# Optimization experiments

Hardware: AMD Instinct MI355X
Metric: run time of the kernel (lower is better)

Reference implementation:

```python
import jax, jax.numpy as jnp
import numpy as np
import math

D_MODEL = 512
N_HEADS = 8
MAX_SPAN = 512
SPAN_LOSS_COEF = 2e-4
NEG_INF = -1.0e9
R_SIZE = 4.0


def soft_span_mask(span, max_span, seq_len):
    # span: (H,) clamped span fractions
    i_idx = jnp.arange(seq_len, dtype=span.dtype)[:, None]
    j_idx = jnp.arange(seq_len, dtype=span.dtype)[None, :]
    dist = i_idx - j_idx                                  # (T, T)
    eff_span = (span * max_span)[:, None, None]           # (H, 1, 1)
    x = eff_span - dist[None, :, :]                       # (H, T, T)
    R = jnp.clip((x + 1.0) / R_SIZE, 0.0, 1.0)
    causal_ok = dist[None, :, :] >= 0
    log_R = jnp.maximum(jnp.log(R + 1e-10), NEG_INF)
    return jnp.where(causal_ok & (R > 0), log_R, NEG_INF)  # (H, T, T)


def setup_inputs() -> dict:
    key = jax.random.key(0)
    ks = jax.random.split(key, 6)
    B, T, D = 4, 2048, D_MODEL
    w_scale = 0.02
    return {
        "x": jax.random.normal(ks[0], (B, T, D), dtype=jnp.float32),
        "wq": jax.random.normal(ks[1], (D, D), dtype=jnp.float32) * w_scale,
        "wk": jax.random.normal(ks[2], (D, D), dtype=jnp.float32) * w_scale,
        "wv": jax.random.normal(ks[3], (D, D), dtype=jnp.float32) * w_scale,
        "wo": jax.random.normal(ks[4], (D, D), dtype=jnp.float32) * w_scale,
        "span_params": jax.random.uniform(ks[5], (N_HEADS,), dtype=jnp.float32),
    }


def reference(x, wq, wk, wv, wo, span_params):
    B, T, D = x.shape
    H = N_HEADS
    d_h = D // H

    clamped_span = jnp.clip(span_params, 0.0, 1.0)

    # nn.Linear(bias=False): y = x @ W.T
    Q = (x @ wq.T).reshape(B, T, H, d_h).transpose(0, 2, 1, 3)  # (B,H,T,dh)
    K = (x @ wk.T).reshape(B, T, H, d_h).transpose(0, 2, 1, 3)
    V = (x @ wv.T).reshape(B, T, H, d_h).transpose(0, 2, 1, 3)

    scale = 1.0 / math.sqrt(d_h)
    scores = jnp.einsum("bhqd,bhkd->bhqk", Q, K) * scale        # (B,H,T,T)
    scores = scores + soft_span_mask(clamped_span, MAX_SPAN, T)[None]

    weights = jax.nn.softmax(scores, axis=-1)
    out = jnp.einsum("bhqk,bhkd->bhqd", weights, V)             # (B,H,T,dh)
    out = out.transpose(0, 2, 1, 3).reshape(B, T, D)
    output = out @ wo.T

    span_loss = SPAN_LOSS_COEF * clamped_span.mean()
    return output, span_loss
```

## Files before the change

kernel.cpp:

```cpp
#include <hip/hip_runtime.h>
#include <math.h>

#define T_SEQ   2048
#define DMODEL  512
#define NHEADS  8
#define DH      64
#define NEG_INF -1.0e9f

typedef __attribute__((ext_vector_type(8))) short short8;
typedef __attribute__((ext_vector_type(4))) float f32x4;
typedef unsigned int u32;
typedef unsigned short u16;

__device__ __forceinline__ u16 f2bf(float f) {
    union { float f; u32 u; } w; w.f = f;
    return (u16)((w.u + 0x8000u) >> 16);
}

__device__ __forceinline__ void async_load16(const u16* g, u16* l) {
    __builtin_amdgcn_global_load_lds(
        (const __attribute__((address_space(1))) u32*)(const void*)g,
        (__attribute__((address_space(3))) u32*)(void*)l, 16, 0, 0);
}

__global__ void cast_all(const float* __restrict__ x,  const float* __restrict__ wq,
                         const float* __restrict__ wk, const float* __restrict__ wv,
                         const float* __restrict__ wo, const float* __restrict__ sp,
                         u16* __restrict__ xb,  u16* __restrict__ wqb,
                         u16* __restrict__ wkb, u16* __restrict__ wvb,
                         u16* __restrict__ wob, float* __restrict__ loss_out)
{
    const int bid = blockIdx.x;
    const float* src; u16* dst; int i;
    if (bid < 4096) { src = x; dst = xb; i = bid * 256 + threadIdx.x; }
    else {
        const int wsel = (bid - 4096) >> 8;
        src = (wsel == 0) ? wq : (wsel == 1) ? wk : (wsel == 2) ? wv : wo;
        dst = (wsel == 0) ? wqb : (wsel == 1) ? wkb : (wsel == 2) ? wvb : wob;
        i = ((bid - 4096) & 255) * 256 + threadIdx.x;
    }
    float4 v = ((const float4*)src)[i];
    ushort4 o;
    o.x = f2bf(v.x); o.y = f2bf(v.y); o.z = f2bf(v.z); o.w = f2bf(v.w);
    ((ushort4*)dst)[i] = o;
    if (bid == 5119 && threadIdx.x == 0) {
        float s = 0.0f;
        for (int h = 0; h < NHEADS; ++h)
            s += fminf(fmaxf(sp[h], 0.0f), 1.0f);
        loss_out[0] = 2e-4f * (s * 0.125f);
    }
}

__global__ __launch_bounds__(256)
void gemm_bf16(const u16* __restrict__ A,
               const u16* __restrict__ W0, const u16* __restrict__ W1,
               const u16* __restrict__ W2,
               u16* __restrict__ Cb0, u16* __restrict__ Cb1,
               u16* __restrict__ Cb2,
               float* __restrict__ Cf, int scatter)
{
    constexpr int K = 512, BK = 64;
    const u16* W  = (blockIdx.z == 0) ? W0 : (blockIdx.z == 1) ? W1 : W2;
    u16*       Cb = (blockIdx.z == 0) ? Cb0 : (blockIdx.z == 1) ? Cb1 : Cb2;

    __shared__ __align__(16) u16 smem[16384];
    u16* As = smem;
    u16* Bs = smem + 8192;

    const int t    = threadIdx.x;
    const int lane = t & 63;
    const int wave = t >> 6;
    const int wm   = wave >> 1, wn = wave & 1;
    const int m0   = blockIdx.x * 128, n0 = blockIdx.y * 128;

    const int srow = t >> 3;
    const int kb   = (t & 7) ^ (srow & 7);
    const u16* gA = A + (size_t)(m0 + srow) * K + kb * 8;
    const u16* gW = W + (size_t)(n0 + srow) * K + kb * 8;

    const int rA = wm * 64 + (lane & 15);
    const int rB = wn * 64 + (lane & 15);
    const int kq = lane >> 4;
    const int offA0 = rA * BK + ((kq      ^ (rA & 7)) * 8);
    const int offA1 = rA * BK + (((4 + kq) ^ (rA & 7)) * 8);
    const int offB0 = rB * BK + ((kq      ^ (rB & 7)) * 8);
    const int offB1 = rB * BK + (((4 + kq) ^ (rB & 7)) * 8);

    f32x4 acc[4][4];
#pragma unroll
    for (int it = 0; it < 4; ++it)
#pragma unroll
        for (int jt = 0; jt < 4; ++jt) acc[it][jt] = (f32x4)0.0f;

    for (int k0 = 0; k0 < K; k0 += BK) {
        __syncthreads();
#pragma unroll
        for (int i = 0; i < 4; ++i) {
            async_load16(gA + k0 + i * (32 * K), As + t * 8 + i * 2048);
            async_load16(gW + k0 + i * (32 * K), Bs + t * 8 + i * 2048);
        }
        __syncthreads();

        short8 af[4][2], bfr[4][2];
#pragma unroll
        for (int it = 0; it < 4; ++it) {
            af[it][0]  = *(const short8*)(As + offA0 + it * 16 * BK);
            af[it][1]  = *(const short8*)(As + offA1 + it * 16 * BK);
            bfr[it][0] = *(const short8*)(Bs + offB0 + it * 16 * BK);
            bfr[it][1] = *(const short8*)(Bs + offB1 + it * 16 * BK);
        }
#pragma unroll
        for (int it = 0; it < 4; ++it)
#pragma unroll
            for (int jt = 0; jt < 4; ++jt) {
                acc[it][jt] = __builtin_amdgcn_mfma_f32_16x16x32_bf16(
                    af[it][0], bfr[jt][0], acc[it][jt], 0, 0, 0);
                acc[it][jt] = __builtin_amdgcn_mfma_f32_16x16x32_bf16(
                    af[it][1], bfr[jt][1], acc[it][jt], 0, 0, 0);
            }
    }

    const int r0 = (lane >> 4) * 4;
    const int cl = lane & 15;

    if (scatter) {
        const bool vt_mode = (blockIdx.z == 2);
        constexpr int P = 136;
#pragma unroll
        for (int rnd = 0; rnd < 2; ++rnd) {
            __syncthreads();
#pragma unroll
            for (int s = 0; s < 2; ++s) {
                const int it = rnd * 2 + s;
                const int lrow = wm * 32 + s * 16 + r0;
#pragma unroll
                for (int jt = 0; jt < 4; ++jt) {
                    const int cc = wn * 64 + jt * 16 + cl;
#pragma unroll
                    for (int r = 0; r < 4; ++r)
                        smem[(lrow + r) * P + cc] = f2bf(acc[it][jt][r]);
                }
            }
            __syncthreads();
            if (!vt_mode) {
                const int lrow2 = t >> 2;
                const int h2    = (t >> 1) & 1;
                const int dhalf = t & 1;
                const int grow  = m0 + (lrow2 >> 5) * 64 + rnd * 32 + (lrow2 & 31);
                const int b     = grow >> 11, tt = grow & 2047;
                const int h     = (n0 >> 6) + h2;
                u16* dst = Cb + ((size_t)((b * NHEADS + h) * T_SEQ + tt)) * DH + dhalf * 32;
                const u16* srcl = smem + lrow2 * P + h2 * 64 + dhalf * 32;
#pragma unroll
                for (int i = 0; i < 4; ++i)
                    ((uint4*)dst)[i] = *(const uint4*)(srcl + i * 8);
            } else {
                const int hd   = t >> 1;
                const int run  = t & 1;
                const int h    = (n0 >> 6) + (hd >> 6);
                const int d    = hd & 63;
                const int tb   = m0 + run * 64 + rnd * 32;
                const int b    = tb >> 11;
                u16* dst = Cb + (((size_t)(b * NHEADS + h) * DH + d) << 11) + (tb & 2047);
                union { uint4 v[4]; u16 s[32]; } pk;
#pragma unroll
                for (int i = 0; i < 32; ++i)
                    pk.s[i] = smem[(run * 32 + i) * P + hd];
#pragma unroll
                for (int i = 0; i < 4; ++i)
                    ((uint4*)dst)[i] = pk.v[i];
            }
        }
    } else {
#pragma unroll
        for (int it = 0; it < 4; ++it) {
#pragma unroll
            for (int r = 0; r < 4; ++r) {
                const int row = m0 + wm * 64 + it * 16 + r0 + r;
#pragma unroll
                for (int jt = 0; jt < 4; ++jt) {
                    const int col = n0 + wn * 64 + jt * 16 + cl;
                    Cf[(size_t)row * DMODEL + col] = acc[it][jt][r];
                }
            }
        }
    }
}

__global__ __launch_bounds__(64, 2)
void attn_wave(const u16* __restrict__ Q, const u16* __restrict__ K,
               const u16* __restrict__ Vt, const float* __restrict__ span_params,
               u16* __restrict__ out)
{
    __shared__ __align__(16) u16 Ps[16 * 72];

    const int lane = threadIdx.x;
    const int nl   = lane & 15;
    const int quad = lane >> 4;
    const int xi   = blockIdx.x;
    const int b    = xi >> 3;
    const int h    = ((xi & 7) + 5 * b) & 7;
    const int bh   = b * NHEADS + h;
    const int q0   = blockIdx.y * 16;

    const u16* Qh = Q  + (size_t)bh * (T_SEQ * DH);
    const u16* Kh = K  + (size_t)bh * (T_SEQ * DH);
    const u16* Vh = Vt + (size_t)bh * (DH * T_SEQ);

    float span = span_params[h];
    span = fminf(fmaxf(span, 0.0f), 1.0f);
    const float eff_span = span * 512.0f;
    const int wspan = (int)(eff_span + 1.0f) + 1;

    short8 qf0 = *(const short8*)(Qh + (size_t)(q0 + nl) * DH + quad * 8);
    short8 qf1 = *(const short8*)(Qh + (size_t)(q0 + nl) * DH + 32 + quad * 8);

    f32x4 o[4];
    float m_r[4], l_r[4];
#pragma unroll
    for (int d = 0; d < 4; ++d) o[d] = (f32x4)0.0f;
#pragma unroll
    for (int r = 0; r < 4; ++r) { m_r[r] = -1.0e30f; l_r[r] = 0.0f; }

    int j_lo = q0 - wspan;
    if (j_lo < 0) j_lo = 0;
    j_lo &= ~63;
    const int j_hi = (q0 + 15) & ~63;

    for (int j0 = j_lo; j0 <= j_hi; j0 += 64) {
        bool any[4];
#pragma unroll
        for (int n = 0; n < 4; ++n) {
            const int jn = j0 + n * 16;
            any[n] = (jn <= q0 + 15) &&
                     ((float)(q0 - jn - 15) < eff_span + 1.0f);
        }

        f32x4 s[4];
#pragma unroll
        for (int n = 0; n < 4; ++n) {
            s[n] = (f32x4)0.0f;
            if (any[n]) {
                const u16* kp = Kh + (size_t)(j0 + n * 16 + nl) * DH + quad * 8;
                short8 b0 = *(const short8*)kp;
                short8 b1 = *(const short8*)(kp + 32);
                s[n] = __builtin_amdgcn_mfma_f32_16x16x32_bf16(qf0, b0, s[n], 0, 0, 0);
                s[n] = __builtin_amdgcn_mfma_f32_16x16x32_bf16(qf1, b1, s[n], 0, 0, 0);
            }
        }

        const bool kf0 = any[0] | any[1];
        const bool kf1 = any[2] | any[3];
        short8 vb0[4], vb1[4];
#pragma unroll
        for (int d = 0; d < 4; ++d) {
            const u16* vp = Vh + (size_t)(d * 16 + nl) * T_SEQ + j0 + quad * 8;
            if (kf0) vb0[d] = *(const short8*)vp;
            if (kf1) vb1[d] = *(const short8*)(vp + 32);
        }

        float tmax[4] = {-1.0e30f, -1.0e30f, -1.0e30f, -1.0e30f};
#pragma unroll
        for (int n = 0; n < 4; ++n) {
            if (!any[n]) continue;
            const int jn = j0 + n * 16;
            const bool causal_b = (jn + 15 > q0);
            const bool span_b   = ((float)(q0 + 15 - jn) > eff_span - 3.0f);
            if (!causal_b && !span_b) {
#pragma unroll
                for (int r = 0; r < 4; ++r) {
                    const float sv = s[n][r] * 0.125f;
                    s[n][r] = sv;
                    tmax[r] = fmaxf(tmax[r], sv);
                }
            } else if (!span_b) {
#pragma unroll
                for (int r = 0; r < 4; ++r) {
                    const int dist = (q0 + quad * 4 + r) - (jn + nl);
                    const float sv = (dist >= 0) ? s[n][r] * 0.125f : NEG_INF;
                    s[n][r] = sv;
                    tmax[r] = fmaxf(tmax[r], sv);
                }
            } else {
#pragma unroll
                for (int r = 0; r < 4; ++r) {
                    const int dist = (q0 + quad * 4 + r) - (jn + nl);
                    float sv = NEG_INF;
                    if (dist >= 0) {
                        float xv = eff_span - (float)dist;
                        float R  = fminf(fmaxf((xv + 1.0f) * 0.25f, 0.0f), 1.0f);
                        if (R > 0.0f)
                            sv = s[n][r] * 0.125f +
                                 ((R < 1.0f) ? __logf(R + 1e-10f) : 0.0f);
                    }
                    s[n][r] = sv;
                    tmax[r] = fmaxf(tmax[r], sv);
                }
            }
        }

        float alpha[4];
#pragma unroll
        for (int r = 0; r < 4; ++r) {
            float t = tmax[r];
            t = fmaxf(t, __shfl_xor(t, 1));
            t = fmaxf(t, __shfl_xor(t, 2));
            t = fmaxf(t, __shfl_xor(t, 4));
            t = fmaxf(t, __shfl_xor(t, 8));
            const float m_new = fmaxf(m_r[r], t);
            alpha[r] = __expf(m_r[r] - m_new);
            m_r[r] = m_new;
        }

        float psum[4] = {0.0f, 0.0f, 0.0f, 0.0f};
#pragma unroll
        for (int n = 0; n < 4; ++n) {
            if (any[n]) {
#pragma unroll
                for (int r = 0; r < 4; ++r) {
                    const float pv = __expf(s[n][r] - m_r[r]);
                    psum[r] += pv;
                    Ps[(quad * 4 + r) * 72 + n * 16 + nl] = f2bf(pv);
                }
            } else {
#pragma unroll
                for (int r = 0; r < 4; ++r)
                    Ps[(quad * 4 + r) * 72 + n * 16 + nl] = 0;
            }
        }
#pragma unroll
        for (int r = 0; r < 4; ++r) {
            float ps = psum[r];
            ps += __shfl_xor(ps, 1);
            ps += __shfl_xor(ps, 2);
            ps += __shfl_xor(ps, 4);
            ps += __shfl_xor(ps, 8);
            l_r[r] = l_r[r] * alpha[r] + ps;
#pragma unroll
            for (int d = 0; d < 4; ++d) o[d][r] *= alpha[r];
        }

        const u16* pb = Ps + nl * 72;
        short8 a0 = *(const short8*)(pb + quad * 8);
        short8 a1 = *(const short8*)(pb + 32 + quad * 8);
#pragma unroll
        for (int d = 0; d < 4; ++d) {
            if (kf0)
                o[d] = __builtin_amdgcn_mfma_f32_16x16x32_bf16(a0, vb0[d], o[d], 0, 0, 0);
            if (kf1)
                o[d] = __builtin_amdgcn_mfma_f32_16x16x32_bf16(a1, vb1[d], o[d], 0, 0, 0);
        }
    }

#pragma unroll
    for (int r = 0; r < 4; ++r) {
        const int qg = q0 + quad * 4 + r;
        const float inv_l = 1.0f / l_r[r];
        u16* op = out + (size_t)(b * T_SEQ + qg) * DMODEL + h * 64;
#pragma unroll
        for (int d = 0; d < 4; ++d)
            op[d * 16 + nl] = f2bf(o[d][r] * inv_l);
    }
}

extern "C" void kernel_launch(void* const* d_in, const int* in_sizes, int n_in,
                              void* d_out, int out_size, void* d_ws, size_t ws_size,
                              hipStream_t stream)
{
    (void)in_sizes; (void)n_in; (void)out_size; (void)ws_size;
    const float* x  = (const float*)d_in[0];
    const float* wq = (const float*)d_in[1];
    const float* wk = (const float*)d_in[2];
    const float* wv = (const float*)d_in[3];
    const float* wo = (const float*)d_in[4];
    const float* sp = (const float*)d_in[5];
    float* out = (float*)d_out;

    const size_t elems = (size_t)4 * T_SEQ * DMODEL;
    u16* xb  = (u16*)d_ws;
    u16* Qb  = xb  + elems;
    u16* Kb  = Qb  + elems;
    u16* Vtb = Kb  + elems;
    u16* Ab  = Vtb + elems;
    u16* wqb = Ab  + elems;
    u16* wkb = wqb + 262144;
    u16* wvb = wkb + 262144;
    u16* wob = wvb + 262144;

    cast_all<<<5120, 256, 0, stream>>>(x, wq, wk, wv, wo, sp,
                                       xb, wqb, wkb, wvb, wob, out + elems);
    gemm_bf16<<<dim3(64, 4, 3), 256, 0, stream>>>(
        xb, wqb, wkb, wvb, Qb, Kb, Vtb, nullptr, 1);
    attn_wave<<<dim3(32, 128), 64, 0, stream>>>(Qb, Kb, Vtb, sp, Ab);
    gemm_bf16<<<dim3(64, 4, 1), 256, 0, stream>>>(
        Ab, wob, wob, wob, nullptr, nullptr, nullptr, out, 0);
}
```

Before: 176.4 us.

## Compute V transposed via swapped GEMM operands and pack four query waves per attention block

The V projection now runs as a separate GEMM with the operands swapped (Wv times x^T). Its output tile is already in the d-by-T orientation, so the epilogue writes contiguous 16-byte runs instead of gathering a strided column out of shared memory. The attention kernel now uses 256-thread blocks of four independent waves, each with its own P buffer, covering 64 queries. Blocks are issued in reverse query order so the longer causal tiles start first. This adds a kernel launch, and the V GEMM leans on indexing assumptions about the tile layout.

```diff
diff --git a/kernel.cpp b/kernel.cpp
--- a/kernel.cpp
+++ b/kernel.cpp
@@ -54,14 +54,12 @@
 __global__ __launch_bounds__(256)
 void gemm_bf16(const u16* __restrict__ A,
                const u16* __restrict__ W0, const u16* __restrict__ W1,
-               const u16* __restrict__ W2,
                u16* __restrict__ Cb0, u16* __restrict__ Cb1,
-               u16* __restrict__ Cb2,
-               float* __restrict__ Cf, int scatter)
+               float* __restrict__ Cf, int mode)
 {
     constexpr int K = 512, BK = 64;
-    const u16* W  = (blockIdx.z == 0) ? W0 : (blockIdx.z == 1) ? W1 : W2;
-    u16*       Cb = (blockIdx.z == 0) ? Cb0 : (blockIdx.z == 1) ? Cb1 : Cb2;
+    const u16* W  = (blockIdx.z == 0) ? W0 : W1;
+    u16*       Cb = (blockIdx.z == 0) ? Cb0 : Cb1;
 
     __shared__ __align__(16) u16 smem[16384];
     u16* As = smem;
@@ -123,55 +121,7 @@
     const int r0 = (lane >> 4) * 4;
     const int cl = lane & 15;
 
-    if (scatter) {
-        const bool vt_mode = (blockIdx.z == 2);
-        constexpr int P = 136;
-#pragma unroll
-        for (int rnd = 0; rnd < 2; ++rnd) {
-            __syncthreads();
-#pragma unroll
-            for (int s = 0; s < 2; ++s) {
-                const int it = rnd * 2 + s;
-                const int lrow = wm * 32 + s * 16 + r0;
-#pragma unroll
-                for (int jt = 0; jt < 4; ++jt) {
-                    const int cc = wn * 64 + jt * 16 + cl;
-#pragma unroll
-                    for (int r = 0; r < 4; ++r)
-                        smem[(lrow + r) * P + cc] = f2bf(acc[it][jt][r]);
-                }
-            }
-            __syncthreads();
-            if (!vt_mode) {
-                const int lrow2 = t >> 2;
-                const int h2    = (t >> 1) & 1;
-                const int dhalf = t & 1;
-                const int grow  = m0 + (lrow2 >> 5) * 64 + rnd * 32 + (lrow2 & 31);
-                const int b     = grow >> 11, tt = grow & 2047;
-                const int h     = (n0 >> 6) + h2;
-                u16* dst = Cb + ((size_t)((b * NHEADS + h) * T_SEQ + tt)) * DH + dhalf * 32;
-                const u16* srcl = smem + lrow2 * P + h2 * 64 + dhalf * 32;
-#pragma unroll
-                for (int i = 0; i < 4; ++i)
-                    ((uint4*)dst)[i] = *(const uint4*)(srcl + i * 8);
-            } else {
-                const int hd   = t >> 1;
-                const int run  = t & 1;
-                const int h    = (n0 >> 6) + (hd >> 6);
-                const int d    = hd & 63;
-                const int tb   = m0 + run * 64 + rnd * 32;
-                const int b    = tb >> 11;
-                u16* dst = Cb + (((size_t)(b * NHEADS + h) * DH + d) << 11) + (tb & 2047);
-                union { uint4 v[4]; u16 s[32]; } pk;
-#pragma unroll
-                for (int i = 0; i < 32; ++i)
-                    pk.s[i] = smem[(run * 32 + i) * P + hd];
-#pragma unroll
-                for (int i = 0; i < 4; ++i)
-                    ((uint4*)dst)[i] = pk.v[i];
-            }
-        }
-    } else {
+    if (mode == 2) {
 #pragma unroll
         for (int it = 0; it < 4; ++it) {
 #pragma unroll
@@ -184,24 +134,72 @@
                 }
             }
         }
-    }
-}
-
-__global__ __launch_bounds__(64, 2)
+        return;
+    }
+
+    constexpr int P = 136;
+#pragma unroll
+    for (int rnd = 0; rnd < 2; ++rnd) {
+        __syncthreads();
+#pragma unroll
+        for (int s = 0; s < 2; ++s) {
+            const int it = rnd * 2 + s;
+            const int lrow = wm * 32 + s * 16 + r0;
+#pragma unroll
+            for (int jt = 0; jt < 4; ++jt) {
+                const int cc = wn * 64 + jt * 16 + cl;
+#pragma unroll
+                for (int r = 0; r < 4; ++r)
+                    smem[(lrow + r) * P + cc] = f2bf(acc[it][jt][r]);
+            }
+        }
+        __syncthreads();
+        if (mode == 0) {
+            const int lrow2 = t >> 2;
+            const int h2    = (t >> 1) & 1;
+            const int dhalf = t & 1;
+            const int grow  = m0 + (lrow2 >> 5) * 64 + rnd * 32 + (lrow2 & 31);
+            const int b     = grow >> 11, tt = grow & 2047;
+            const int h     = (n0 >> 6) + h2;
+            u16* dst = Cb + ((size_t)((b * NHEADS + h) * T_SEQ + tt)) * DH + dhalf * 32;
+            const u16* srcl = smem + lrow2 * P + h2 * 64 + dhalf * 32;
+#pragma unroll
+            for (int i = 0; i < 4; ++i)
+                ((uint4*)dst)[i] = *(const uint4*)(srcl + i * 8);
+        } else {
+            const int rl = t >> 2;
+            const int q  = t & 3;
+            const int m  = m0 + (rl >> 5) * 64 + rnd * 32 + (rl & 31);
+            const int h  = m >> 6, d = m & 63;
+            const int n  = n0 + q * 32;
+            const int b  = n >> 11;
+            u16* dst = Cb + (((size_t)(b * NHEADS + h) * DH + d) << 11) + (n & 2047);
+            const u16* srcl = smem + rl * P + q * 32;
+            ((uint4*)dst)[0] = *(const uint4*)(srcl);
+            ((uint4*)dst)[1] = *(const uint4*)(srcl + 8);
+            ((uint4*)dst)[2] = *(const uint4*)(srcl + 16);
+            ((uint4*)dst)[3] = *(const uint4*)(srcl + 24);
+        }
+    }
+}
+
+__global__ __launch_bounds__(256)
 void attn_wave(const u16* __restrict__ Q, const u16* __restrict__ K,
                const u16* __restrict__ Vt, const float* __restrict__ span_params,
                u16* __restrict__ out)
 {
-    __shared__ __align__(16) u16 Ps[16 * 72];
-
-    const int lane = threadIdx.x;
+    __shared__ __align__(16) u16 Ps[4][16 * 72];
+
+    const int tid  = threadIdx.x;
+    const int lane = tid & 63;
+    const int w    = tid >> 6;
     const int nl   = lane & 15;
     const int quad = lane >> 4;
     const int xi   = blockIdx.x;
     const int b    = xi >> 3;
     const int h    = ((xi & 7) + 5 * b) & 7;
     const int bh   = b * NHEADS + h;
-    const int q0   = blockIdx.y * 16;
+    const int q0   = (31 - (int)blockIdx.y) * 64 + w * 16;
 
     const u16* Qh = Q  + (size_t)bh * (T_SEQ * DH);
     const u16* Kh = K  + (size_t)bh * (T_SEQ * DH);
@@ -320,12 +318,12 @@
                 for (int r = 0; r < 4; ++r) {
                     const float pv = __expf(s[n][r] - m_r[r]);
                     psum[r] += pv;
-                    Ps[(quad * 4 + r) * 72 + n * 16 + nl] = f2bf(pv);
+                    Ps[w][(quad * 4 + r) * 72 + n * 16 + nl] = f2bf(pv);
                 }
             } else {
 #pragma unroll
                 for (int r = 0; r < 4; ++r)
-                    Ps[(quad * 4 + r) * 72 + n * 16 + nl] = 0;
+                    Ps[w][(quad * 4 + r) * 72 + n * 16 + nl] = 0;
             }
         }
 #pragma unroll
@@ -340,7 +338,7 @@
             for (int d = 0; d < 4; ++d) o[d][r] *= alpha[r];
         }
 
-        const u16* pb = Ps + nl * 72;
+        const u16* pb = Ps[w] + nl * 72;
         short8 a0 = *(const short8*)(pb + quad * 8);
         short8 a1 = *(const short8*)(pb + 32 + quad * 8);
 #pragma unroll
@@ -389,9 +387,11 @@
 
     cast_all<<<5120, 256, 0, stream>>>(x, wq, wk, wv, wo, sp,
                                        xb, wqb, wkb, wvb, wob, out + elems);
-    gemm_bf16<<<dim3(64, 4, 3), 256, 0, stream>>>(
-        xb, wqb, wkb, wvb, Qb, Kb, Vtb, nullptr, 1);
-    attn_wave<<<dim3(32, 128), 64, 0, stream>>>(Qb, Kb, Vtb, sp, Ab);
+    gemm_bf16<<<dim3(64, 4, 2), 256, 0, stream>>>(
+        xb, wqb, wkb, Qb, Kb, nullptr, 0);
+    gemm_bf16<<<dim3(4, 64, 1), 256, 0, stream>>>(
+        wvb, xb, nullptr, Vtb, nullptr, nullptr, 1);
+    attn_wave<<<dim3(32, 32), 256, 0, stream>>>(Qb, Kb, Vtb, sp, Ab);
     gemm_bf16<<<dim3(64, 4, 1), 256, 0, stream>>>(
-        Ab, wob, wob, wob, nullptr, nullptr, nullptr, out, 0);
-}
+        Ab, wob, nullptr, nullptr, nullptr, out, 2);
+}
```

Measured after the change: 189.3 us. +7.3%, slower.
